# Kernel optimization log

Measured on AMD Instinct MI355X. Metric: run time of the kernel, lower is better.

The kernel has to match this reference:

```python
import jax, jax.numpy as jnp
import numpy as np

T, B, D, H, L = 512, 64, 1024, 1024, 2
W_SCALE = 0.02  # keep tanh out of saturation


def setup_inputs() -> dict:
    key = jax.random.key(0)
    ks = jax.random.split(key, 7)
    return {
        "x": jax.random.normal(ks[0], (T, B, D), dtype=jnp.float32),
        "Wi": jax.random.normal(ks[1], (L, H, D), dtype=jnp.float32) * W_SCALE,
        "bi": jax.random.normal(ks[2], (L, H), dtype=jnp.float32) * W_SCALE,
        "Wh": jax.random.normal(ks[3], (L, H, H), dtype=jnp.float32) * W_SCALE,
        "bh": jax.random.normal(ks[4], (L, H), dtype=jnp.float32) * W_SCALE,
        "Wo": jax.random.normal(ks[5], (L, H, H), dtype=jnp.float32) * W_SCALE,
        "bo": jax.random.normal(ks[6], (L, H), dtype=jnp.float32) * W_SCALE,
    }


def reference(x, Wi, bi, Wh, bh, Wo, bo):
    # Faithful to the original: ONE hidden state shared across all layers,
    # overwritten by each RNNCell call within a timestep.
    num_layers = Wi.shape[0]
    batch = x.shape[1]
    hidden0 = jnp.zeros((batch, Wh.shape[-1]), dtype=x.dtype)

    def step(hidden, xt):
        out = xt
        for l in range(num_layers):
            # h = i2h(out) + h2h(hidden); o = h2o(h); new hidden = tanh(h)
            h = out @ Wi[l].T + bi[l] + hidden @ Wh[l].T + bh[l]  # [B,H]
            out = h @ Wo[l].T + bo[l]
            hidden = jnp.tanh(h)
        return hidden, out

    final_hidden, outs = jax.lax.scan(step, hidden0, x)  # outs: [T,B,H]
    return outs, final_hidden
```

## Files before the change

### kernel.cpp

```cpp
#include <hip/hip_runtime.h>
#include <cstdint>
#include <cstddef>

#define TT   512
#define NWG  512
#define SLOT 65536
#define FINALOFF ((size_t)TT * (size_t)SLOT)

#define OFF_M     0
#define OFF_H0    2097152
#define OFF_TH0   (OFF_H0 + 131072)
#define OFF_H1A   (OFF_TH0 + 131072)
#define OFF_H1B   (OFF_H1A + 131072)
#define OFF_TH1   (OFF_H1B + 131072)
#define OFF_Z0    (OFF_TH1 + 131072)
#define OFF_Z1    (OFF_Z0 + 131072)
#define OFF_B0    (OFF_Z1 + 131072)
#define OFF_C1    (OFF_B0 + 4096)
#define OFF_CF    (OFF_C1 + 4096)
#define OFF_AF    (OFF_CF + 4096)

typedef _Float16 f16;
typedef unsigned long long ull;
typedef _Float16 v8h __attribute__((ext_vector_type(8)));
typedef float v4f __attribute__((ext_vector_type(4)));

union U2 { ull u[2]; v8h v; };

__device__ __forceinline__ void st2(void* p, f16 v) {
  __hip_atomic_store((unsigned short*)p, __builtin_bit_cast(unsigned short, v),
                     __ATOMIC_RELAXED, __HIP_MEMORY_SCOPE_AGENT);
}
__device__ __forceinline__ f16 ld2(const void* p) {
  unsigned short u = __hip_atomic_load((const unsigned short*)p,
                                       __ATOMIC_RELAXED, __HIP_MEMORY_SCOPE_AGENT);
  return __builtin_bit_cast(f16, u);
}
__device__ __forceinline__ ull ld8(const void* p) {
  return __hip_atomic_load((const ull*)p, __ATOMIC_RELAXED, __HIP_MEMORY_SCOPE_AGENT);
}

__device__ __forceinline__ float rcpf(float x) {
#if __has_builtin(__builtin_amdgcn_rcpf)
  return __builtin_amdgcn_rcpf(x);
#else
  return 1.0f / x;
#endif
}
__device__ __forceinline__ float tanhfast(float x) {
  x = fminf(fmaxf(x, -20.0f), 20.0f);
  const float u = __expf(-2.0f * x);
  return 1.0f - 2.0f * u * rcpf(1.0f + u);
}

__global__ void k_init(unsigned int* flags) {
  flags[blockIdx.x * 1024 + threadIdx.x] = 0u;
}

__global__ void k_bias(const float* __restrict__ Wi, const float* __restrict__ bi,
                       const float* __restrict__ bh, const float* __restrict__ bo,
                       float* __restrict__ b0, float* __restrict__ c1) {
  const int i = blockIdx.x * 256 + threadIdx.x;
  const float* row = Wi + 1048576 + (size_t)i * 1024;
  float s = 0.f;
  for (int k = 0; k < 1024; k += 4) {
    const float4 w = *(const float4*)&row[k];
    const float4 v = *(const float4*)&bo[k];
    s += w.x * v.x + w.y * v.y + w.z * v.z + w.w * v.w;
  }
  c1[i] = s + bi[1024 + i] + bh[1024 + i];
  b0[i] = bi[i] + bh[i];
}

__global__ __launch_bounds__(256) void k_gemm_M(const float* __restrict__ Wi,
                                                const float* __restrict__ Wo,
                                                f16* __restrict__ Mh) {
  const float* A = Wi + 1048576;
  const float* B = Wo;
  __shared__ float As[16][68];
  __shared__ float Bs[16][68];
  const int bi = blockIdx.x >> 4, bj = blockIdx.x & 15;
  const int i0 = bi * 64, d0 = bj * 64;
  const int ti = threadIdx.x >> 4, tj = threadIdx.x & 15;
  float acc[4][4] = {};
  for (int kc = 0; kc < 1024; kc += 16) {
    const int r = threadIdx.x >> 2, cg = (threadIdx.x & 3) << 2;
    const float4 av = *(const float4*)&A[(size_t)(i0 + r) * 1024 + kc + cg];
    As[cg + 0][r] = av.x; As[cg + 1][r] = av.y; As[cg + 2][r] = av.z; As[cg + 3][r] = av.w;
    const int c2 = threadIdx.x >> 4, dg = (threadIdx.x & 15) << 2;
    const float4 bv = *(const float4*)&B[(size_t)(kc + c2) * 1024 + d0 + dg];
    *(float4*)&Bs[c2][dg] = bv;
    __syncthreads();
#pragma unroll
    for (int kk = 0; kk < 16; ++kk) {
      float a[4], b[4];
#pragma unroll
      for (int q = 0; q < 4; ++q) { a[q] = As[kk][ti * 4 + q]; b[q] = Bs[kk][tj * 4 + q]; }
#pragma unroll
      for (int p = 0; p < 4; ++p)
#pragma unroll
        for (int q = 0; q < 4; ++q) acc[p][q] += a[p] * b[q];
    }
    __syncthreads();
  }
#pragma unroll
  for (int p = 0; p < 4; ++p)
#pragma unroll
    for (int q = 0; q < 4; ++q)
      Mh[(size_t)(i0 + ti * 4 + p) * 1024 + (size_t)(d0 + tj * 4 + q)] = (f16)acc[p][q];
}

__device__ __forceinline__ void ld_frags(const f16* base, v8h out[8]) {
  ull u0[8], u1[8];
#pragma unroll
  for (int s = 0; s < 8; ++s) { const f16* p = base + s * 32; u0[s] = ld8(p); u1[s] = ld8(p + 4); }
#pragma unroll
  for (int s = 0; s < 8; ++s) { U2 c; c.u[0] = u0[s]; c.u[1] = u1[s]; out[s] = c.v; }
}

__global__ __launch_bounds__(256, 2) void k_rnn(
    const float* __restrict__ x,
    const float* __restrict__ Wi, const float* __restrict__ Wh,
    const float* __restrict__ Wo, const float* __restrict__ bo,
    char* __restrict__ ws, float* __restrict__ dout)
{
  const f16* Mh  = (const f16*)(ws + OFF_M);
  f16* h0h  = (f16*)(ws + OFF_H0);
  f16* th0h = (f16*)(ws + OFF_TH0);
  f16* h1b[2] = { (f16*)(ws + OFF_H1A), (f16*)(ws + OFF_H1B) };
  f16* th1h = (f16*)(ws + OFF_TH1);
  f16* zb[2] = { (f16*)(ws + OFF_Z0), (f16*)(ws + OFF_Z1) };
  const float* b0p = (const float*)(ws + OFF_B0);
  const float* c1p = (const float*)(ws + OFF_C1);

  const int wg = blockIdx.x;
  const bool is_aux = (wg >= 256);
  const int p = is_aux ? (wg - 256) : wg;
  const int bq = p & 3;
  const int jt = p >> 2;
  const int j0 = jt * 16;
  const int tid = threadIdx.x;
  const int l = tid & 63, w = tid >> 6;
  const int lj = l & 15, lk = l >> 4;
  const int jrow = j0 + lj;
  const int rb = tid >> 4, rj = tid & 15;

  unsigned int* gfC = (unsigned int*)(ws + OFF_CF) + bq * 256;
  unsigned int* gfA = (unsigned int*)(ws + OFF_AF) + bq * 256;

  __shared__ __align__(16) f16 WiL[16 * 1032];
  __shared__ float red[1024];

  const size_t actbase = (size_t)(bq * 16 + lj) * 1024 + (size_t)(w * 256 + lk * 8);
  const int redw = w * 256 + lk * 64 + lj;
  const size_t rdst = (size_t)(bq * 16 + rb) * 1024 + (size_t)(j0 + rj);

  if (!is_aux) {
    v8h wWh0[8], wM[8], wWh1[8];
#pragma unroll
    for (int s = 0; s < 8; ++s) {
      const int k0 = w * 256 + s * 32 + lk * 8;
      {
        const float* pp = &Wh[(size_t)jrow * 1024 + k0];
        float4 a = *(const float4*)pp, b = *(const float4*)(pp + 4);
        wWh0[s] = (v8h){(f16)a.x,(f16)a.y,(f16)a.z,(f16)a.w,(f16)b.x,(f16)b.y,(f16)b.z,(f16)b.w};
      }
      {
        const float* pp = &Wh[1048576 + (size_t)jrow * 1024 + k0];
        float4 a = *(const float4*)pp, b = *(const float4*)(pp + 4);
        wWh1[s] = (v8h){(f16)a.x,(f16)a.y,(f16)a.z,(f16)a.w,(f16)b.x,(f16)b.y,(f16)b.z,(f16)b.w};
      }
      wM[s] = *(const v8h*)&Mh[(size_t)jrow * 1024 + k0];
    }
    const float c1v = c1p[j0 + rj];

    for (int t = 0; t < TT; ++t) {
      const unsigned int cthA = 2u * t;
      const unsigned int athA = (t == 0) ? 1u : (unsigned int)t;
      if (tid < 64) {
        while (__hip_atomic_load(&gfC[tid * 4], __ATOMIC_RELAXED, __HIP_MEMORY_SCOPE_AGENT) < cthA)
          __builtin_amdgcn_s_sleep(1);
      } else if (tid < 128) {
        while (__hip_atomic_load(&gfA[(tid - 64) * 4], __ATOMIC_RELAXED, __HIP_MEMORY_SCOPE_AGENT) < athA)
          __builtin_amdgcn_s_sleep(1);
      }
      __syncthreads();

      const f16 zv = ld2(&zb[t & 1][rdst]);
      v4f acc = {0.f, 0.f, 0.f, 0.f};
      if (t > 0) {
        v8h thf[8];
        ld_frags(th1h + actbase, thf);
#pragma unroll
        for (int s = 0; s < 8; ++s)
          acc = __builtin_amdgcn_mfma_f32_16x16x32_f16(thf[s], wWh0[s], acc, 0, 0, 0);
      }
#pragma unroll
      for (int q = 0; q < 4; ++q) red[redw + q * 16] = acc[q];
      __syncthreads();
      const float h0 = red[tid] + red[256 + tid] + red[512 + tid] + red[768 + tid] + (float)zv;
      st2(&h0h[rdst], (f16)h0);
      st2(&th0h[rdst], (f16)tanhfast(h0));
      asm volatile("s_waitcnt vmcnt(0)" ::: "memory");
      __syncthreads();
      if (tid == 0)
        __hip_atomic_store(&gfC[jt * 4], 2u * t + 1u, __ATOMIC_RELAXED, __HIP_MEMORY_SCOPE_AGENT);

      if (tid < 64) {
        while (__hip_atomic_load(&gfC[tid * 4], __ATOMIC_RELAXED, __HIP_MEMORY_SCOPE_AGENT) < 2u * t + 1u)
          __builtin_amdgcn_s_sleep(1);
      }
      __syncthreads();

      v8h g0f[8], t0f[8];
      ld_frags(h0h + actbase, g0f);
      ld_frags(th0h + actbase, t0f);
      v4f aM = {0.f, 0.f, 0.f, 0.f}, aW = {0.f, 0.f, 0.f, 0.f};
#pragma unroll
      for (int s = 0; s < 8; ++s) {
        aM = __builtin_amdgcn_mfma_f32_16x16x32_f16(g0f[s], wM[s], aM, 0, 0, 0);
        aW = __builtin_amdgcn_mfma_f32_16x16x32_f16(t0f[s], wWh1[s], aW, 0, 0, 0);
      }
#pragma unroll
      for (int q = 0; q < 4; ++q) red[redw + q * 16] = aM[q] + aW[q];
      __syncthreads();
      const float h1 = red[tid] + red[256 + tid] + red[512 + tid] + red[768 + tid] + c1v;
      const float th1v = tanhfast(h1);
      st2(&h1b[t & 1][rdst], (f16)h1);
      st2(&th1h[rdst], (f16)th1v);
      if (t == TT - 1) dout[FINALOFF + rdst] = th1v;
      asm volatile("s_waitcnt vmcnt(0)" ::: "memory");
      __syncthreads();
      if (tid == 0)
        __hip_atomic_store(&gfC[jt * 4], 2u * t + 2u, __ATOMIC_RELAXED, __HIP_MEMORY_SCOPE_AGENT);
    }
  } else {
    v8h wWo1[8];
#pragma unroll
    for (int s = 0; s < 8; ++s) {
      const int k0 = w * 256 + s * 32 + lk * 8;
      const float* pp = &Wo[1048576 + (size_t)jrow * 1024 + k0];
      float4 a = *(const float4*)pp, b = *(const float4*)(pp + 4);
      wWo1[s] = (v8h){(f16)a.x,(f16)a.y,(f16)a.z,(f16)a.w,(f16)b.x,(f16)b.y,(f16)b.z,(f16)b.w};
    }
    for (int u = tid; u < 4096; u += 256) {
      const int rr = u >> 8, c4 = (u & 255) << 2;
      const float4 v = *(const float4*)&Wi[(size_t)(j0 + rr) * 1024 + c4];
      f16* dst = &WiL[rr * 1032 + c4];
      dst[0] = (f16)v.x; dst[1] = (f16)v.y; dst[2] = (f16)v.z; dst[3] = (f16)v.w;
    }
    const float b0v = b0p[j0 + rj];
    const float bo1v = bo[1024 + j0 + rj];
    __syncthreads();

    auto z1c = [&](const float* xt, f16* zdst) {
      __syncthreads();
      v4f acc = {0.f, 0.f, 0.f, 0.f};
#pragma unroll
      for (int s = 0; s < 8; ++s) {
        const float* pp = xt + actbase + s * 32;
        const float4 a = *(const float4*)pp;
        const float4 b = *(const float4*)(pp + 4);
        const v8h af = {(f16)a.x,(f16)a.y,(f16)a.z,(f16)a.w,
                        (f16)b.x,(f16)b.y,(f16)b.z,(f16)b.w};
        const v8h bf = *(const v8h*)&WiL[lj * 1032 + w * 256 + s * 32 + lk * 8];
        acc = __builtin_amdgcn_mfma_f32_16x16x32_f16(af, bf, acc, 0, 0, 0);
      }
#pragma unroll
      for (int q = 0; q < 4; ++q) red[redw + q * 16] = acc[q];
      __syncthreads();
      const float r = red[tid] + red[256 + tid] + red[512 + tid] + red[768 + tid] + b0v;
      st2(&zdst[rdst], (f16)r);
    };

    z1c(x, zb[0]);
    z1c(x + SLOT, zb[1]);
    asm volatile("s_waitcnt vmcnt(0)" ::: "memory");
    __syncthreads();
    if (tid == 0)
      __hip_atomic_store(&gfA[jt * 4], 1u, __ATOMIC_RELAXED, __HIP_MEMORY_SCOPE_AGENT);

    for (int i = 1; i <= TT; ++i) {
      if (tid < 64) {
        while (__hip_atomic_load(&gfC[tid * 4], __ATOMIC_RELAXED, __HIP_MEMORY_SCOPE_AGENT) < 2u * i)
          __builtin_amdgcn_s_sleep(1);
      }
      __syncthreads();

      v8h hrf[8];
      ld_frags(h1b[(i - 1) & 1] + actbase, hrf);
      v4f a2 = {0.f, 0.f, 0.f, 0.f};
#pragma unroll
      for (int s = 0; s < 8; ++s)
        a2 = __builtin_amdgcn_mfma_f32_16x16x32_f16(hrf[s], wWo1[s], a2, 0, 0, 0);
#pragma unroll
      for (int q = 0; q < 4; ++q) red[redw + q * 16] = a2[q];
      __syncthreads();
      const float s1 = red[tid] + red[256 + tid] + red[512 + tid] + red[768 + tid] + bo1v;
      dout[(size_t)(i - 1) * SLOT + rdst] = s1;

      if (i + 1 < TT) z1c(x + (size_t)(i + 1) * SLOT, zb[(i + 1) & 1]);

      asm volatile("s_waitcnt vmcnt(0)" ::: "memory");
      __syncthreads();
      if (tid == 0)
        __hip_atomic_store(&gfA[jt * 4], (unsigned int)(i + 1), __ATOMIC_RELAXED, __HIP_MEMORY_SCOPE_AGENT);
    }
  }
}

extern "C" void kernel_launch(void* const* d_in, const int* in_sizes, int n_in,
                              void* d_out, int out_size, void* d_ws, size_t ws_size,
                              hipStream_t stream) {
  (void)in_sizes; (void)n_in; (void)out_size; (void)ws_size;
  const float* x  = (const float*)d_in[0];
  const float* Wi = (const float*)d_in[1];
  const float* bi = (const float*)d_in[2];
  const float* Wh = (const float*)d_in[3];
  const float* bh = (const float*)d_in[4];
  const float* Wo = (const float*)d_in[5];
  const float* bo = (const float*)d_in[6];
  char* ws = (char*)d_ws;
  float* out = (float*)d_out;

  k_init<<<2, 1024, 0, stream>>>((unsigned int*)(ws + OFF_CF));
  k_bias<<<4, 256, 0, stream>>>(Wi, bi, bh, bo, (float*)(ws + OFF_B0), (float*)(ws + OFF_C1));
  k_gemm_M<<<256, 256, 0, stream>>>(Wi, Wo, (f16*)(ws + OFF_M));
  k_rnn<<<NWG, 256, 0, stream>>>(x, Wi, Wh, Wo, bo, ws, out);
}
```

Baseline: 6.437 ms.

## Replace per-WG flag polling with atomic counters and deepen z/h1 ring buffers

Cross-workgroup synchronization used to poll 64 per-workgroup flags with 64 threads. It now uses one fetch-add counter per batch quarter, polled by a single thread. The z and h1 double buffers become 4-deep rings, so the aux workgroups can produce input projections three steps ahead and the main chain waits on them less. The aux loop also issues the global loads of x before waiting, hiding their latency. The risk is contention on the atomic counters and more workspace.

```diff
diff --git a/kernel.cpp b/kernel.cpp
--- a/kernel.cpp
+++ b/kernel.cpp
@@ -8,17 +8,14 @@
 #define FINALOFF ((size_t)TT * (size_t)SLOT)
 
 #define OFF_M     0
-#define OFF_H0    2097152
+#define OFF_H1R   2097152
+#define OFF_TH1   (OFF_H1R + 4*131072)
+#define OFF_H0    (OFF_TH1 + 131072)
 #define OFF_TH0   (OFF_H0 + 131072)
-#define OFF_H1A   (OFF_TH0 + 131072)
-#define OFF_H1B   (OFF_H1A + 131072)
-#define OFF_TH1   (OFF_H1B + 131072)
-#define OFF_Z0    (OFF_TH1 + 131072)
-#define OFF_Z1    (OFF_Z0 + 131072)
-#define OFF_B0    (OFF_Z1 + 131072)
+#define OFF_ZR    (OFF_TH0 + 131072)
+#define OFF_B0    (OFF_ZR + 4*131072)
 #define OFF_C1    (OFF_B0 + 4096)
-#define OFF_CF    (OFF_C1 + 4096)
-#define OFF_AF    (OFF_CF + 4096)
+#define OFF_CNT   (OFF_C1 + 4096)
 
 typedef _Float16 f16;
 typedef unsigned long long ull;
@@ -38,6 +35,13 @@
 }
 __device__ __forceinline__ ull ld8(const void* p) {
   return __hip_atomic_load((const ull*)p, __ATOMIC_RELAXED, __HIP_MEMORY_SCOPE_AGENT);
+}
+__device__ __forceinline__ void poll_ge(const unsigned int* c, unsigned int tgt) {
+  while (__hip_atomic_load(c, __ATOMIC_RELAXED, __HIP_MEMORY_SCOPE_AGENT) < tgt)
+    __builtin_amdgcn_s_sleep(1);
+}
+__device__ __forceinline__ void cnt_add(unsigned int* c) {
+  __hip_atomic_fetch_add(c, 1u, __ATOMIC_RELAXED, __HIP_MEMORY_SCOPE_AGENT);
 }
 
 __device__ __forceinline__ float rcpf(float x) {
@@ -53,8 +57,8 @@
   return 1.0f - 2.0f * u * rcpf(1.0f + u);
 }
 
-__global__ void k_init(unsigned int* flags) {
-  flags[blockIdx.x * 1024 + threadIdx.x] = 0u;
+__global__ void k_init(unsigned int* cnt) {
+  if (threadIdx.x < 384) cnt[threadIdx.x] = 0u;
 }
 
 __global__ void k_bias(const float* __restrict__ Wi, const float* __restrict__ bi,
@@ -125,11 +129,13 @@
     char* __restrict__ ws, float* __restrict__ dout)
 {
   const f16* Mh  = (const f16*)(ws + OFF_M);
+  f16* h1r[4] = { (f16*)(ws + OFF_H1R), (f16*)(ws + OFF_H1R + 131072),
+                  (f16*)(ws + OFF_H1R + 2*131072), (f16*)(ws + OFF_H1R + 3*131072) };
+  f16* th1h = (f16*)(ws + OFF_TH1);
   f16* h0h  = (f16*)(ws + OFF_H0);
   f16* th0h = (f16*)(ws + OFF_TH0);
-  f16* h1b[2] = { (f16*)(ws + OFF_H1A), (f16*)(ws + OFF_H1B) };
-  f16* th1h = (f16*)(ws + OFF_TH1);
-  f16* zb[2] = { (f16*)(ws + OFF_Z0), (f16*)(ws + OFF_Z1) };
+  f16* zr[4] = { (f16*)(ws + OFF_ZR), (f16*)(ws + OFF_ZR + 131072),
+                 (f16*)(ws + OFF_ZR + 2*131072), (f16*)(ws + OFF_ZR + 3*131072) };
   const float* b0p = (const float*)(ws + OFF_B0);
   const float* c1p = (const float*)(ws + OFF_C1);
 
@@ -145,8 +151,9 @@
   const int jrow = j0 + lj;
   const int rb = tid >> 4, rj = tid & 15;
 
-  unsigned int* gfC = (unsigned int*)(ws + OFF_CF) + bq * 256;
-  unsigned int* gfA = (unsigned int*)(ws + OFF_AF) + bq * 256;
+  unsigned int* cntA = (unsigned int*)(ws + OFF_CNT) + bq * 96;
+  unsigned int* cntB = cntA + 32;
+  unsigned int* cntX = cntA + 64;
 
   __shared__ __align__(16) f16 WiL[16 * 1032];
   __shared__ float red[1024];
@@ -172,21 +179,18 @@
       }
       wM[s] = *(const v8h*)&Mh[(size_t)jrow * 1024 + k0];
     }
+#pragma unroll
+    for (int s = 0; s < 8; ++s) {
+      asm volatile("" : "+v"(wWh0[s]), "+v"(wM[s]), "+v"(wWh1[s]));
+    }
     const float c1v = c1p[j0 + rj];
 
     for (int t = 0; t < TT; ++t) {
-      const unsigned int cthA = 2u * t;
-      const unsigned int athA = (t == 0) ? 1u : (unsigned int)t;
-      if (tid < 64) {
-        while (__hip_atomic_load(&gfC[tid * 4], __ATOMIC_RELAXED, __HIP_MEMORY_SCOPE_AGENT) < cthA)
-          __builtin_amdgcn_s_sleep(1);
-      } else if (tid < 128) {
-        while (__hip_atomic_load(&gfA[(tid - 64) * 4], __ATOMIC_RELAXED, __HIP_MEMORY_SCOPE_AGENT) < athA)
-          __builtin_amdgcn_s_sleep(1);
-      }
-      __syncthreads();
-
-      const f16 zv = ld2(&zb[t & 1][rdst]);
+      if (tid == 0)      poll_ge(cntB, 64u * (unsigned)t);
+      else if (tid == 1) poll_ge(cntX, 64u * (t >= 3 ? (unsigned)(t - 2) : 1u));
+      __syncthreads();
+
+      const f16 zv = ld2(&zr[t & 3][rdst]);
       v4f acc = {0.f, 0.f, 0.f, 0.f};
       if (t > 0) {
         v8h thf[8];
@@ -203,13 +207,9 @@
       st2(&th0h[rdst], (f16)tanhfast(h0));
       asm volatile("s_waitcnt vmcnt(0)" ::: "memory");
       __syncthreads();
-      if (tid == 0)
-        __hip_atomic_store(&gfC[jt * 4], 2u * t + 1u, __ATOMIC_RELAXED, __HIP_MEMORY_SCOPE_AGENT);
-
-      if (tid < 64) {
-        while (__hip_atomic_load(&gfC[tid * 4], __ATOMIC_RELAXED, __HIP_MEMORY_SCOPE_AGENT) < 2u * t + 1u)
-          __builtin_amdgcn_s_sleep(1);
-      }
+      if (tid == 0) cnt_add(cntA);
+
+      if (tid == 0) poll_ge(cntA, 64u * (unsigned)(t + 1));
       __syncthreads();
 
       v8h g0f[8], t0f[8];
@@ -225,14 +225,13 @@
       for (int q = 0; q < 4; ++q) red[redw + q * 16] = aM[q] + aW[q];
       __syncthreads();
       const float h1 = red[tid] + red[256 + tid] + red[512 + tid] + red[768 + tid] + c1v;
+      st2(&h1r[t & 3][rdst], (f16)h1);
       const float th1v = tanhfast(h1);
-      st2(&h1b[t & 1][rdst], (f16)h1);
       st2(&th1h[rdst], (f16)th1v);
       if (t == TT - 1) dout[FINALOFF + rdst] = th1v;
       asm volatile("s_waitcnt vmcnt(0)" ::: "memory");
       __syncthreads();
-      if (tid == 0)
-        __hip_atomic_store(&gfC[jt * 4], 2u * t + 2u, __ATOMIC_RELAXED, __HIP_MEMORY_SCOPE_AGENT);
+      if (tid == 0) cnt_add(cntB);
     }
   } else {
     v8h wWo1[8];
@@ -243,6 +242,8 @@
       float4 a = *(const float4*)pp, b = *(const float4*)(pp + 4);
       wWo1[s] = (v8h){(f16)a.x,(f16)a.y,(f16)a.z,(f16)a.w,(f16)b.x,(f16)b.y,(f16)b.z,(f16)b.w};
     }
+#pragma unroll
+    for (int s = 0; s < 8; ++s) { asm volatile("" : "+v"(wWo1[s])); }
     for (int u = tid; u < 4096; u += 256) {
       const int rr = u >> 8, c4 = (u & 255) << 2;
       const float4 v = *(const float4*)&Wi[(size_t)(j0 + rr) * 1024 + c4];
@@ -253,9 +254,9 @@
     const float bo1v = bo[1024 + j0 + rj];
     __syncthreads();
 
-    auto z1c = [&](const float* xt, f16* zdst) {
-      __syncthreads();
-      v4f acc = {0.f, 0.f, 0.f, 0.f};
+    auto zmake = [&](const float* xt, f16* zdst) {
+      __syncthreads();
+      v4f az = {0.f, 0.f, 0.f, 0.f};
 #pragma unroll
       for (int s = 0; s < 8; ++s) {
         const float* pp = xt + actbase + s * 32;
@@ -264,31 +265,40 @@
         const v8h af = {(f16)a.x,(f16)a.y,(f16)a.z,(f16)a.w,
                         (f16)b.x,(f16)b.y,(f16)b.z,(f16)b.w};
         const v8h bf = *(const v8h*)&WiL[lj * 1032 + w * 256 + s * 32 + lk * 8];
-        acc = __builtin_amdgcn_mfma_f32_16x16x32_f16(af, bf, acc, 0, 0, 0);
-      }
-#pragma unroll
-      for (int q = 0; q < 4; ++q) red[redw + q * 16] = acc[q];
+        az = __builtin_amdgcn_mfma_f32_16x16x32_f16(af, bf, az, 0, 0, 0);
+      }
+#pragma unroll
+      for (int q = 0; q < 4; ++q) red[redw + q * 16] = az[q];
       __syncthreads();
       const float r = red[tid] + red[256 + tid] + red[512 + tid] + red[768 + tid] + b0v;
       st2(&zdst[rdst], (f16)r);
     };
 
-    z1c(x, zb[0]);
-    z1c(x + SLOT, zb[1]);
+    zmake(x, zr[0]);
+    zmake(x + SLOT, zr[1]);
+    zmake(x + 2 * (size_t)SLOT, zr[2]);
+    zmake(x + 3 * (size_t)SLOT, zr[3]);
     asm volatile("s_waitcnt vmcnt(0)" ::: "memory");
     __syncthreads();
-    if (tid == 0)
-      __hip_atomic_store(&gfA[jt * 4], 1u, __ATOMIC_RELAXED, __HIP_MEMORY_SCOPE_AGENT);
+    if (tid == 0) cnt_add(cntX);
 
     for (int i = 1; i <= TT; ++i) {
-      if (tid < 64) {
-        while (__hip_atomic_load(&gfC[tid * 4], __ATOMIC_RELAXED, __HIP_MEMORY_SCOPE_AGENT) < 2u * i)
-          __builtin_amdgcn_s_sleep(1);
-      }
+      const bool dz = (i + 3 <= TT - 1);
+      float4 xa[8], xb[8];
+      if (dz) {
+        const float* xt = x + (size_t)(i + 3) * SLOT;
+#pragma unroll
+        for (int s = 0; s < 8; ++s) {
+          const float* pp = xt + actbase + s * 32;
+          xa[s] = *(const float4*)pp;
+          xb[s] = *(const float4*)(pp + 4);
+        }
+      }
+      if (tid == 0) poll_ge(cntB, 64u * (unsigned)i);
       __syncthreads();
 
       v8h hrf[8];
-      ld_frags(h1b[(i - 1) & 1] + actbase, hrf);
+      ld_frags(h1r[(i - 1) & 3] + actbase, hrf);
       v4f a2 = {0.f, 0.f, 0.f, 0.f};
 #pragma unroll
       for (int s = 0; s < 8; ++s)
@@ -299,12 +309,26 @@
       const float s1 = red[tid] + red[256 + tid] + red[512 + tid] + red[768 + tid] + bo1v;
       dout[(size_t)(i - 1) * SLOT + rdst] = s1;
 
-      if (i + 1 < TT) z1c(x + (size_t)(i + 1) * SLOT, zb[(i + 1) & 1]);
+      if (dz) {
+        __syncthreads();
+        v4f az = {0.f, 0.f, 0.f, 0.f};
+#pragma unroll
+        for (int s = 0; s < 8; ++s) {
+          const v8h af = {(f16)xa[s].x,(f16)xa[s].y,(f16)xa[s].z,(f16)xa[s].w,
+                          (f16)xb[s].x,(f16)xb[s].y,(f16)xb[s].z,(f16)xb[s].w};
+          const v8h bf = *(const v8h*)&WiL[lj * 1032 + w * 256 + s * 32 + lk * 8];
+          az = __builtin_amdgcn_mfma_f32_16x16x32_f16(af, bf, az, 0, 0, 0);
+        }
+#pragma unroll
+        for (int q = 0; q < 4; ++q) red[redw + q * 16] = az[q];
+        __syncthreads();
+        const float r = red[tid] + red[256 + tid] + red[512 + tid] + red[768 + tid] + b0v;
+        st2(&zr[(i + 3) & 3][rdst], (f16)r);
+      }
 
       asm volatile("s_waitcnt vmcnt(0)" ::: "memory");
       __syncthreads();
-      if (tid == 0)
-        __hip_atomic_store(&gfA[jt * 4], (unsigned int)(i + 1), __ATOMIC_RELAXED, __HIP_MEMORY_SCOPE_AGENT);
+      if (tid == 0) cnt_add(cntX);
     }
   }
 }
@@ -323,7 +347,7 @@
   char* ws = (char*)d_ws;
   float* out = (float*)d_out;
 
-  k_init<<<2, 1024, 0, stream>>>((unsigned int*)(ws + OFF_CF));
+  k_init<<<1, 512, 0, stream>>>((unsigned int*)(ws + OFF_CNT));
   k_bias<<<4, 256, 0, stream>>>(Wi, bi, bh, bo, (float*)(ws + OFF_B0), (float*)(ws + OFF_C1));
   k_gemm_M<<<256, 256, 0, stream>>>(Wi, Wo, (f16*)(ws + OFF_M));
   k_rnn<<<NWG, 256, 0, stream>>>(x, Wi, Wh, Wo, bo, ws, out);
```

Result: slower. 7.425 ms (+15.3%).

## Precompute layer-0 input projection up front and merge aux workgroups into recurrent kernel

Applied to the files above, without the earlier changes.

The x·Wi0 projection for all timesteps now runs as a separate parallel GEMM kernel before the recurrence, storing fp16 results in the output buffer, which later gets overwritten. The auxiliary workgroups that computed z and the Wo1 output projection are removed. Their output GEMM is folded into the 256 main workgroups, overlapped with the barrier waits, and weights move from registers into LDS. This halves the workgroup count and removes the cross-group aux flag synchronisation from the critical path. The cost is extra per-step work in each main workgroup and LDS weight reads.

```diff
diff --git a/kernel.cpp b/kernel.cpp
--- a/kernel.cpp
+++ b/kernel.cpp
@@ -3,22 +3,20 @@
 #include <cstddef>
 
 #define TT   512
-#define NWG  512
+#define NWG  256
 #define SLOT 65536
+#define SLOTB 262144
 #define FINALOFF ((size_t)TT * (size_t)SLOT)
 
 #define OFF_M     0
 #define OFF_H0    2097152
 #define OFF_TH0   (OFF_H0 + 131072)
-#define OFF_H1A   (OFF_TH0 + 131072)
+#define OFF_TH1   (OFF_TH0 + 131072)
+#define OFF_H1A   (OFF_TH1 + 131072)
 #define OFF_H1B   (OFF_H1A + 131072)
-#define OFF_TH1   (OFF_H1B + 131072)
-#define OFF_Z0    (OFF_TH1 + 131072)
-#define OFF_Z1    (OFF_Z0 + 131072)
-#define OFF_B0    (OFF_Z1 + 131072)
+#define OFF_B0    (OFF_H1B + 131072)
 #define OFF_C1    (OFF_B0 + 4096)
-#define OFF_CF    (OFF_C1 + 4096)
-#define OFF_AF    (OFF_CF + 4096)
+#define OFF_FLAGS (OFF_C1 + 4096)
 
 typedef _Float16 f16;
 typedef unsigned long long ull;
@@ -26,18 +24,21 @@
 typedef float v4f __attribute__((ext_vector_type(4)));
 
 union U2 { ull u[2]; v8h v; };
+union P4 { f16 h[4]; ull u; };
 
 __device__ __forceinline__ void st2(void* p, f16 v) {
   __hip_atomic_store((unsigned short*)p, __builtin_bit_cast(unsigned short, v),
                      __ATOMIC_RELAXED, __HIP_MEMORY_SCOPE_AGENT);
 }
-__device__ __forceinline__ f16 ld2(const void* p) {
-  unsigned short u = __hip_atomic_load((const unsigned short*)p,
-                                       __ATOMIC_RELAXED, __HIP_MEMORY_SCOPE_AGENT);
-  return __builtin_bit_cast(f16, u);
-}
 __device__ __forceinline__ ull ld8(const void* p) {
   return __hip_atomic_load((const ull*)p, __ATOMIC_RELAXED, __HIP_MEMORY_SCOPE_AGENT);
+}
+__device__ __forceinline__ void ld_frags(const f16* base, v8h out[8]) {
+  ull u0[8], u1[8];
+#pragma unroll
+  for (int s = 0; s < 8; ++s) { const f16* p = base + s * 32; u0[s] = ld8(p); u1[s] = ld8(p + 4); }
+#pragma unroll
+  for (int s = 0; s < 8; ++s) { U2 c; c.u[0] = u0[s]; c.u[1] = u1[s]; out[s] = c.v; }
 }
 
 __device__ __forceinline__ float rcpf(float x) {
@@ -54,7 +55,7 @@
 }
 
 __global__ void k_init(unsigned int* flags) {
-  flags[blockIdx.x * 1024 + threadIdx.x] = 0u;
+  flags[threadIdx.x] = 0u;
 }
 
 __global__ void k_bias(const float* __restrict__ Wi, const float* __restrict__ bi,
@@ -110,202 +111,191 @@
       Mh[(size_t)(i0 + ti * 4 + p) * 1024 + (size_t)(d0 + tj * 4 + q)] = (f16)acc[p][q];
 }
 
-__device__ __forceinline__ void ld_frags(const f16* base, v8h out[8]) {
-  ull u0[8], u1[8];
-#pragma unroll
-  for (int s = 0; s < 8; ++s) { const f16* p = base + s * 32; u0[s] = ld8(p); u1[s] = ld8(p + 4); }
-#pragma unroll
-  for (int s = 0; s < 8; ++s) { U2 c; c.u[0] = u0[s]; c.u[1] = u1[s]; out[s] = c.v; }
-}
-
-__global__ __launch_bounds__(256, 2) void k_rnn(
-    const float* __restrict__ x,
-    const float* __restrict__ Wi, const float* __restrict__ Wh,
-    const float* __restrict__ Wo, const float* __restrict__ bo,
+__global__ __launch_bounds__(256, 1) void k_z1(const float* __restrict__ x,
+                                               const float* __restrict__ Wi,
+                                               const float* __restrict__ b0p,
+                                               float* __restrict__ dout) {
+  const int t = blockIdx.x;
+  const int tid = threadIdx.x, l = tid & 63, w = tid >> 6;
+  const int lj = l & 15, lk = l >> 4;
+  __shared__ __align__(16) f16 XL[64 * 1032];
+  const float* xt = x + (size_t)t * SLOT;
+  for (int u = tid; u < 16384; u += 256) {
+    const int b = u >> 8, c4 = (u & 255) << 2;
+    const float4 v = *(const float4*)&xt[(size_t)b * 1024 + c4];
+    P4 p; p.h[0] = (f16)v.x; p.h[1] = (f16)v.y; p.h[2] = (f16)v.z; p.h[3] = (f16)v.w;
+    *(ull*)&XL[b * 1032 + c4] = p.u;
+  }
+  __syncthreads();
+  for (int jt = 0; jt < 16; ++jt) {
+    const int jb = w * 256 + jt * 16;
+    v4f acc[4] = {{0.f,0.f,0.f,0.f},{0.f,0.f,0.f,0.f},{0.f,0.f,0.f,0.f},{0.f,0.f,0.f,0.f}};
+    for (int ks = 0; ks < 32; ++ks) {
+      const int k0 = ks * 32 + lk * 8;
+      const float* p = &Wi[(size_t)(jb + lj) * 1024 + k0];
+      const float4 a = *(const float4*)p, b = *(const float4*)(p + 4);
+      const v8h wf = {(f16)a.x,(f16)a.y,(f16)a.z,(f16)a.w,
+                      (f16)b.x,(f16)b.y,(f16)b.z,(f16)b.w};
+#pragma unroll
+      for (int bt = 0; bt < 4; ++bt) {
+        const v8h xf = *(const v8h*)&XL[(bt * 16 + lj) * 1032 + k0];
+        acc[bt] = __builtin_amdgcn_mfma_f32_16x16x32_f16(xf, wf, acc[bt], 0, 0, 0);
+      }
+    }
+    const float bias = b0p[jb + lj];
+#pragma unroll
+    for (int bt = 0; bt < 4; ++bt)
+#pragma unroll
+      for (int q = 0; q < 4; ++q) {
+        const int b = bt * 16 + lk * 4 + q;
+        f16* dst = (f16*)((char*)dout + (size_t)t * SLOTB + (size_t)(b >> 4) * 65536
+                          + (size_t)(b & 15) * 2048) + (jb + lj);
+        *dst = (f16)(acc[bt][q] + bias);
+      }
+  }
+}
+
+__global__ __launch_bounds__(256, 1) void k_rnn(
+    const float* __restrict__ Wh, const float* __restrict__ Wo,
+    const float* __restrict__ bo,
     char* __restrict__ ws, float* __restrict__ dout)
 {
-  const f16* Mh  = (const f16*)(ws + OFF_M);
+  const f16* Mh = (const f16*)(ws + OFF_M);
   f16* h0h  = (f16*)(ws + OFF_H0);
   f16* th0h = (f16*)(ws + OFF_TH0);
-  f16* h1b[2] = { (f16*)(ws + OFF_H1A), (f16*)(ws + OFF_H1B) };
   f16* th1h = (f16*)(ws + OFF_TH1);
-  f16* zb[2] = { (f16*)(ws + OFF_Z0), (f16*)(ws + OFF_Z1) };
-  const float* b0p = (const float*)(ws + OFF_B0);
+  f16* h1r[2] = { (f16*)(ws + OFF_H1A), (f16*)(ws + OFF_H1B) };
   const float* c1p = (const float*)(ws + OFF_C1);
+  unsigned int* flags = (unsigned int*)(ws + OFF_FLAGS);
 
   const int wg = blockIdx.x;
-  const bool is_aux = (wg >= 256);
-  const int p = is_aux ? (wg - 256) : wg;
-  const int bq = p & 3;
-  const int jt = p >> 2;
+  const int bq = wg & 3;
+  const int jt = wg >> 2;
   const int j0 = jt * 16;
   const int tid = threadIdx.x;
   const int l = tid & 63, w = tid >> 6;
   const int lj = l & 15, lk = l >> 4;
-  const int jrow = j0 + lj;
   const int rb = tid >> 4, rj = tid & 15;
-
-  unsigned int* gfC = (unsigned int*)(ws + OFF_CF) + bq * 256;
-  unsigned int* gfA = (unsigned int*)(ws + OFF_AF) + bq * 256;
-
-  __shared__ __align__(16) f16 WiL[16 * 1032];
+  unsigned int* gf = flags + bq * 64;
+
+  __shared__ __align__(16) char WLb[4 * 32768];
   __shared__ float red[1024];
+
+  {
+    const float* srcs[3] = { Wh, Wh + 1048576, Wo + 1048576 };
+    const int mi[3] = { 0, 2, 3 };
+#pragma unroll
+    for (int m = 0; m < 3; ++m) {
+      const float* src = srcs[m];
+      for (int u = tid; u < 4096; u += 256) {
+        const int j = u >> 8, c4 = (u & 255) << 2;
+        const float4 v = *(const float4*)&src[(size_t)(j0 + j) * 1024 + c4];
+        P4 p; p.h[0] = (f16)v.x; p.h[1] = (f16)v.y; p.h[2] = (f16)v.z; p.h[3] = (f16)v.w;
+        *(ull*)(WLb + mi[m] * 32768 + ((c4 >> 3) << 8) + (j << 4) + ((c4 & 4) << 1)) = p.u;
+      }
+    }
+    for (int u = tid; u < 2048; u += 256) {
+      const int j = u >> 7, c8 = (u & 127) << 3;
+      const v8h mv = *(const v8h*)&Mh[(size_t)(j0 + j) * 1024 + c8];
+      *(v8h*)(WLb + 32768 + ((c8 >> 3) << 8) + (j << 4)) = mv;
+    }
+  }
+  const float c1v = c1p[j0 + rj];
+  const float bo1v = bo[1024 + j0 + rj];
+  __syncthreads();
 
   const size_t actbase = (size_t)(bq * 16 + lj) * 1024 + (size_t)(w * 256 + lk * 8);
   const int redw = w * 256 + lk * 64 + lj;
   const size_t rdst = (size_t)(bq * 16 + rb) * 1024 + (size_t)(j0 + rj);
-
-  if (!is_aux) {
-    v8h wWh0[8], wM[8], wWh1[8];
+  const int fbase = ((w * 32 + lk) << 8) + (lj << 4);
+
+  auto wfrag = [&](int m, int s) -> v8h {
+    return *(const v8h*)(WLb + m * 32768 + fbase + (s << 10));
+  };
+  auto zptr = [&](int t) -> const f16* {
+    return (const f16*)((const char*)dout + (size_t)t * SLOTB + (size_t)bq * 65536
+                        + (size_t)rb * 2048) + (j0 + rj);
+  };
+  auto reduce4 = [&](v4f a) -> float {
+    __syncthreads();
+#pragma unroll
+    for (int q = 0; q < 4; ++q) red[redw + q * 16] = a[q];
+    __syncthreads();
+    return red[tid] + red[256 + tid] + red[512 + tid] + red[768 + tid];
+  };
+  auto arrive = [&](unsigned int ph) {
+    asm volatile("s_waitcnt vmcnt(0)" ::: "memory");
+    __syncthreads();
+    if (tid == 0)
+      __hip_atomic_store(&gf[jt], ph, __ATOMIC_RELAXED, __HIP_MEMORY_SCOPE_AGENT);
+  };
+  auto wait = [&](unsigned int ph) {
+    if (tid < 64)
+      while (__hip_atomic_load(&gf[tid], __ATOMIC_RELAXED, __HIP_MEMORY_SCOPE_AGENT) < ph)
+        __builtin_amdgcn_s_sleep(1);
+    __syncthreads();
+    asm volatile("" ::: "memory");
+  };
+
+  float zv = (float)(*zptr(0));
+  unsigned int ph = 0;
+  v4f a2 = {0.f, 0.f, 0.f, 0.f};
+
+  for (int t = 0; t < TT; ++t) {
+    v8h hrf[8];
+    v4f accA = {0.f, 0.f, 0.f, 0.f};
+    if (t > 0) {
+      v8h thf[8];
+      ld_frags(th1h + actbase, thf);
+      ld_frags(h1r[(t - 1) & 1] + actbase, hrf);
+#pragma unroll
+      for (int s = 0; s < 8; ++s)
+        accA = __builtin_amdgcn_mfma_f32_16x16x32_f16(thf[s], wfrag(0, s), accA, 0, 0, 0);
+    }
+    const float h0 = reduce4(accA) + zv;
+    st2(&h0h[rdst], (f16)h0);
+    st2(&th0h[rdst], (f16)tanhfast(h0));
+    arrive(++ph);
+    float zn = 0.f;
+    if (t + 1 < TT) zn = (float)(*zptr(t + 1));
+    if (t > 0) {
+      v4f aa = {0.f, 0.f, 0.f, 0.f};
+#pragma unroll
+      for (int s = 0; s < 8; ++s)
+        aa = __builtin_amdgcn_mfma_f32_16x16x32_f16(hrf[s], wfrag(3, s), aa, 0, 0, 0);
+      a2 = aa;
+    }
+    wait(ph);
+
+    v8h g0f[8], t0f[8];
+    ld_frags(h0h + actbase, g0f);
+    ld_frags(th0h + actbase, t0f);
+    v4f aM = {0.f, 0.f, 0.f, 0.f}, aW = {0.f, 0.f, 0.f, 0.f};
 #pragma unroll
     for (int s = 0; s < 8; ++s) {
-      const int k0 = w * 256 + s * 32 + lk * 8;
-      {
-        const float* pp = &Wh[(size_t)jrow * 1024 + k0];
-        float4 a = *(const float4*)pp, b = *(const float4*)(pp + 4);
-        wWh0[s] = (v8h){(f16)a.x,(f16)a.y,(f16)a.z,(f16)a.w,(f16)b.x,(f16)b.y,(f16)b.z,(f16)b.w};
-      }
-      {
-        const float* pp = &Wh[1048576 + (size_t)jrow * 1024 + k0];
-        float4 a = *(const float4*)pp, b = *(const float4*)(pp + 4);
-        wWh1[s] = (v8h){(f16)a.x,(f16)a.y,(f16)a.z,(f16)a.w,(f16)b.x,(f16)b.y,(f16)b.z,(f16)b.w};
-      }
-      wM[s] = *(const v8h*)&Mh[(size_t)jrow * 1024 + k0];
-    }
-    const float c1v = c1p[j0 + rj];
-
-    for (int t = 0; t < TT; ++t) {
-      const unsigned int cthA = 2u * t;
-      const unsigned int athA = (t == 0) ? 1u : (unsigned int)t;
-      if (tid < 64) {
-        while (__hip_atomic_load(&gfC[tid * 4], __ATOMIC_RELAXED, __HIP_MEMORY_SCOPE_AGENT) < cthA)
-          __builtin_amdgcn_s_sleep(1);
-      } else if (tid < 128) {
-        while (__hip_atomic_load(&gfA[(tid - 64) * 4], __ATOMIC_RELAXED, __HIP_MEMORY_SCOPE_AGENT) < athA)
-          __builtin_amdgcn_s_sleep(1);
-      }
-      __syncthreads();
-
-      const f16 zv = ld2(&zb[t & 1][rdst]);
-      v4f acc = {0.f, 0.f, 0.f, 0.f};
-      if (t > 0) {
-        v8h thf[8];
-        ld_frags(th1h + actbase, thf);
-#pragma unroll
-        for (int s = 0; s < 8; ++s)
-          acc = __builtin_amdgcn_mfma_f32_16x16x32_f16(thf[s], wWh0[s], acc, 0, 0, 0);
-      }
-#pragma unroll
-      for (int q = 0; q < 4; ++q) red[redw + q * 16] = acc[q];
-      __syncthreads();
-      const float h0 = red[tid] + red[256 + tid] + red[512 + tid] + red[768 + tid] + (float)zv;
-      st2(&h0h[rdst], (f16)h0);
-      st2(&th0h[rdst], (f16)tanhfast(h0));
-      asm volatile("s_waitcnt vmcnt(0)" ::: "memory");
-      __syncthreads();
-      if (tid == 0)
-        __hip_atomic_store(&gfC[jt * 4], 2u * t + 1u, __ATOMIC_RELAXED, __HIP_MEMORY_SCOPE_AGENT);
-
-      if (tid < 64) {
-        while (__hip_atomic_load(&gfC[tid * 4], __ATOMIC_RELAXED, __HIP_MEMORY_SCOPE_AGENT) < 2u * t + 1u)
-          __builtin_amdgcn_s_sleep(1);
-      }
-      __syncthreads();
-
-      v8h g0f[8], t0f[8];
-      ld_frags(h0h + actbase, g0f);
-      ld_frags(th0h + actbase, t0f);
-      v4f aM = {0.f, 0.f, 0.f, 0.f}, aW = {0.f, 0.f, 0.f, 0.f};
-#pragma unroll
-      for (int s = 0; s < 8; ++s) {
-        aM = __builtin_amdgcn_mfma_f32_16x16x32_f16(g0f[s], wM[s], aM, 0, 0, 0);
-        aW = __builtin_amdgcn_mfma_f32_16x16x32_f16(t0f[s], wWh1[s], aW, 0, 0, 0);
-      }
-#pragma unroll
-      for (int q = 0; q < 4; ++q) red[redw + q * 16] = aM[q] + aW[q];
-      __syncthreads();
-      const float h1 = red[tid] + red[256 + tid] + red[512 + tid] + red[768 + tid] + c1v;
-      const float th1v = tanhfast(h1);
-      st2(&h1b[t & 1][rdst], (f16)h1);
-      st2(&th1h[rdst], (f16)th1v);
-      if (t == TT - 1) dout[FINALOFF + rdst] = th1v;
-      asm volatile("s_waitcnt vmcnt(0)" ::: "memory");
-      __syncthreads();
-      if (tid == 0)
-        __hip_atomic_store(&gfC[jt * 4], 2u * t + 2u, __ATOMIC_RELAXED, __HIP_MEMORY_SCOPE_AGENT);
-    }
-  } else {
-    v8h wWo1[8];
-#pragma unroll
-    for (int s = 0; s < 8; ++s) {
-      const int k0 = w * 256 + s * 32 + lk * 8;
-      const float* pp = &Wo[1048576 + (size_t)jrow * 1024 + k0];
-      float4 a = *(const float4*)pp, b = *(const float4*)(pp + 4);
-      wWo1[s] = (v8h){(f16)a.x,(f16)a.y,(f16)a.z,(f16)a.w,(f16)b.x,(f16)b.y,(f16)b.z,(f16)b.w};
-    }
-    for (int u = tid; u < 4096; u += 256) {
-      const int rr = u >> 8, c4 = (u & 255) << 2;
-      const float4 v = *(const float4*)&Wi[(size_t)(j0 + rr) * 1024 + c4];
-      f16* dst = &WiL[rr * 1032 + c4];
-      dst[0] = (f16)v.x; dst[1] = (f16)v.y; dst[2] = (f16)v.z; dst[3] = (f16)v.w;
-    }
-    const float b0v = b0p[j0 + rj];
-    const float bo1v = bo[1024 + j0 + rj];
-    __syncthreads();
-
-    auto z1c = [&](const float* xt, f16* zdst) {
-      __syncthreads();
-      v4f acc = {0.f, 0.f, 0.f, 0.f};
-#pragma unroll
-      for (int s = 0; s < 8; ++s) {
-        const float* pp = xt + actbase + s * 32;
-        const float4 a = *(const float4*)pp;
-        const float4 b = *(const float4*)(pp + 4);
-        const v8h af = {(f16)a.x,(f16)a.y,(f16)a.z,(f16)a.w,
-                        (f16)b.x,(f16)b.y,(f16)b.z,(f16)b.w};
-        const v8h bf = *(const v8h*)&WiL[lj * 1032 + w * 256 + s * 32 + lk * 8];
-        acc = __builtin_amdgcn_mfma_f32_16x16x32_f16(af, bf, acc, 0, 0, 0);
-      }
-#pragma unroll
-      for (int q = 0; q < 4; ++q) red[redw + q * 16] = acc[q];
-      __syncthreads();
-      const float r = red[tid] + red[256 + tid] + red[512 + tid] + red[768 + tid] + b0v;
-      st2(&zdst[rdst], (f16)r);
-    };
-
-    z1c(x, zb[0]);
-    z1c(x + SLOT, zb[1]);
-    asm volatile("s_waitcnt vmcnt(0)" ::: "memory");
-    __syncthreads();
-    if (tid == 0)
-      __hip_atomic_store(&gfA[jt * 4], 1u, __ATOMIC_RELAXED, __HIP_MEMORY_SCOPE_AGENT);
-
-    for (int i = 1; i <= TT; ++i) {
-      if (tid < 64) {
-        while (__hip_atomic_load(&gfC[tid * 4], __ATOMIC_RELAXED, __HIP_MEMORY_SCOPE_AGENT) < 2u * i)
-          __builtin_amdgcn_s_sleep(1);
-      }
-      __syncthreads();
-
-      v8h hrf[8];
-      ld_frags(h1b[(i - 1) & 1] + actbase, hrf);
-      v4f a2 = {0.f, 0.f, 0.f, 0.f};
-#pragma unroll
-      for (int s = 0; s < 8; ++s)
-        a2 = __builtin_amdgcn_mfma_f32_16x16x32_f16(hrf[s], wWo1[s], a2, 0, 0, 0);
-#pragma unroll
-      for (int q = 0; q < 4; ++q) red[redw + q * 16] = a2[q];
-      __syncthreads();
-      const float s1 = red[tid] + red[256 + tid] + red[512 + tid] + red[768 + tid] + bo1v;
-      dout[(size_t)(i - 1) * SLOT + rdst] = s1;
-
-      if (i + 1 < TT) z1c(x + (size_t)(i + 1) * SLOT, zb[(i + 1) & 1]);
-
-      asm volatile("s_waitcnt vmcnt(0)" ::: "memory");
-      __syncthreads();
-      if (tid == 0)
-        __hip_atomic_store(&gfA[jt * 4], (unsigned int)(i + 1), __ATOMIC_RELAXED, __HIP_MEMORY_SCOPE_AGENT);
-    }
+      aM = __builtin_amdgcn_mfma_f32_16x16x32_f16(g0f[s], wfrag(1, s), aM, 0, 0, 0);
+      aW = __builtin_amdgcn_mfma_f32_16x16x32_f16(t0f[s], wfrag(2, s), aW, 0, 0, 0);
+    }
+    const float h1 = reduce4(aM + aW) + c1v;
+    const float th1v = tanhfast(h1);
+    st2(&h1r[t & 1][rdst], (f16)h1);
+    st2(&th1h[rdst], (f16)th1v);
+    if (t == TT - 1) dout[FINALOFF + rdst] = th1v;
+    arrive(++ph);
+    if (t > 0)
+      dout[(size_t)(t - 1) * SLOT + rdst] = reduce4(a2) + bo1v;
+    wait(ph);
+    zv = zn;
+  }
+
+  {
+    v8h hrf[8];
+    ld_frags(h1r[(TT - 1) & 1] + actbase, hrf);
+    v4f aa = {0.f, 0.f, 0.f, 0.f};
+#pragma unroll
+    for (int s = 0; s < 8; ++s)
+      aa = __builtin_amdgcn_mfma_f32_16x16x32_f16(hrf[s], wfrag(3, s), aa, 0, 0, 0);
+    dout[(size_t)(TT - 1) * SLOT + rdst] = reduce4(aa) + bo1v;
   }
 }
 
@@ -323,8 +313,9 @@
   char* ws = (char*)d_ws;
   float* out = (float*)d_out;
 
-  k_init<<<2, 1024, 0, stream>>>((unsigned int*)(ws + OFF_CF));
+  k_init<<<1, 256, 0, stream>>>((unsigned int*)(ws + OFF_FLAGS));
   k_bias<<<4, 256, 0, stream>>>(Wi, bi, bh, bo, (float*)(ws + OFF_B0), (float*)(ws + OFF_C1));
   k_gemm_M<<<256, 256, 0, stream>>>(Wi, Wo, (f16*)(ws + OFF_M));
-  k_rnn<<<NWG, 256, 0, stream>>>(x, Wi, Wh, Wo, bo, ws, out);
-}
+  k_z1<<<512, 256, 0, stream>>>(x, Wi, (const float*)(ws + OFF_B0), out);
+  k_rnn<<<NWG, 256, 0, stream>>>(Wh, Wo, bo, ws, out);
+}
```

New measurement: 6.255 ms. -2.8%, faster.
